# Kernel optimization log

Hardware: AMD Instinct MI355X
Metric: run time of the kernel (lower is better)

Reference implementation:

```python
import jax, jax.numpy as jnp
import numpy as np
import math

B, C_GT, H, W = 32, 1, 256, 1216
SH, SW = 16, 48  # samplesH, samplesW (eval-mode jitter fixed at 0)


def _gauss_kernel():
    # kernel_size = [int(2H/(SH+1)), int(2W/(SW+1))], sigma = size/3 (per original code)
    kh = int(2 * H / (SH + 1))
    kw = int(2 * W / (SW + 1))
    sh = 2 * H / (SH + 1) / 3.0
    sw = 2 * W / (SW + 1) / 3.0
    gh = np.exp(-(((np.arange(kh) - (kh - 1) / 2) / sh) ** 2) / 2) / (sh * math.sqrt(2 * math.pi))
    gw = np.exp(-(((np.arange(kw) - (kw - 1) / 2) / sw) ** 2) / 2) / (sw * math.sqrt(2 * math.pi))
    k = np.outer(gh, gw)
    k = k / k.sum()
    return jnp.asarray(k, jnp.float32)


def _grid_sample_bilinear(img, grid):
    # img [B,C,H,W]; grid [B,Hs,Ws,2] with (x,y) in [-1,1].
    # Matches F.grid_sample(mode='bilinear', padding_mode='zeros', align_corners=False).
    Bb, C, Hh, Ww = img.shape
    x = (grid[..., 0] + 1.0) * Ww / 2.0 - 0.5
    y = (grid[..., 1] + 1.0) * Hh / 2.0 - 0.5
    x0 = jnp.floor(x); y0 = jnp.floor(y)
    x1 = x0 + 1.0;     y1 = y0 + 1.0
    wx1 = x - x0; wx0 = 1.0 - wx1
    wy1 = y - y0; wy0 = 1.0 - wy1
    imt = img.transpose(0, 2, 3, 1)  # [B,H,W,C]
    bidx = jnp.arange(Bb)[:, None, None]

    def gather(yc, xc, wgt):
        m = (yc >= 0) & (yc <= Hh - 1) & (xc >= 0) & (xc <= Ww - 1)
        yi = jnp.clip(yc, 0, Hh - 1).astype(jnp.int32)
        xi = jnp.clip(xc, 0, Ww - 1).astype(jnp.int32)
        v = imt[bidx, yi, xi]  # [B,Hs,Ws,C]
        return v * (wgt * m)[..., None]

    out = (gather(y0, x0, wy0 * wx0) + gather(y0, x1, wy0 * wx1)
           + gather(y1, x0, wy1 * wx0) + gather(y1, x1, wy1 * wx1))
    return out.transpose(0, 3, 1, 2)  # [B,C,Hs,Ws]


def _forward(gt, dense_vector_field):
    # GaussianSmooth: grouped VALID conv with a big separable Gaussian kernel
    k = _gauss_kernel()
    kern = jnp.broadcast_to(k[None, None], (2, 1, k.shape[0], k.shape[1]))
    smoothed = jax.lax.conv_general_dilated(dense_vector_field, kern, (1, 1), 'VALID',
                                            feature_group_count=2)  # [B,2,H',W']
    # F.interpolate(mode='nearest') to (SH, SW): idx = floor(i * in / out)
    hi = np.arange(SH) * smoothed.shape[2] // SH
    wi = np.arange(SW) * smoothed.shape[3] // SW
    svf = smoothed[:, :, hi][:, :, :, wi]  # [B,2,SH,SW]

    # WarpSample base grid (x first, then y — grid_sample convention)
    gw, gh = np.meshgrid(np.linspace(-(SW - 1) / SW, (SW - 1) / SW, SW),
                         np.linspace(-(SH - 1) / SH, (SH - 1) / SH, SH))
    norm_grid = jnp.asarray(np.stack((gw, gh), 2), jnp.float32)  # [SH,SW,2]
    grid_to_sample = svf.transpose(0, 2, 3, 1) + norm_grid  # [B,SH,SW,2]

    gt_sampled = _grid_sample_bilinear(gt, grid_to_sample)  # [B,1,SH,SW]

    # expand(): vectorized scatter replacing the per-pixel Python loop.
    row = jnp.clip(((grid_to_sample[..., 1] + 1.0) / 2.0 * H).astype(jnp.int32), 0, H - 1)
    col = jnp.clip(((grid_to_sample[..., 0] + 1.0) / 2.0 * W).astype(jnp.int32), 0, W - 1)
    bidx = jnp.arange(gt.shape[0])[:, None, None]
    sparse = jnp.zeros((gt.shape[0], H, W, gt.shape[1]), gt.dtype)
    sparse = sparse.at[bidx, row, col].set(gt_sampled.transpose(0, 2, 3, 1))
    sparse = sparse.transpose(0, 3, 1, 2)  # [B,1,H,W]
    # eval-mode KITTI: zero the top 96 rows (no LiDAR returns there)
    sparse = sparse.at[:, :, 0:96, :].set(0.0)
    return sparse, dense_vector_field.transpose(0, 2, 3, 1), grid_to_sample


def setup_inputs():
    key = jax.random.key(0)
    k1, k2 = jax.random.split(key)
    gt = jax.random.uniform(k1, (B, C_GT, H, W), dtype=jnp.float32) * 80.0  # KITTI depth range
    dense_vector_field = jax.random.normal(k2, (B, 2, H, W), dtype=jnp.float32) * 0.1
    return {"gt": gt, "dense_vector_field": dense_vector_field}


def reference(gt, dense_vector_field):
    return _forward(gt, dense_vector_field)
```

## Files before the change

kernel.cpp:

```cpp
#include <hip/hip_runtime.h>
#include <math.h>

#ifndef M_PI
#define M_PI 3.14159265358979323846
#endif

#define Hh   256
#define Ww   1216
#define HWsz (Hh * Ww)
#define Bb   32
#define KH   30
#define KW   49
#define NTAP (KH * KW)
#define SHs  16
#define SWs  48
#define NPB  (SHs * SWs)
#define NPTS (Bb * NPB)
#define OUT0 (Bb * HWsz)
#define OUT1 (Bb * HWsz * 2)

__device__ __forceinline__ float samp4(const float* __restrict__ g, float yc, float xc, float w) {
#pragma clang fp contract(off)
    bool m = (yc >= 0.0f) && (yc <= 255.0f) && (xc >= 0.0f) && (xc <= 1215.0f);
    float ycl = fminf(fmaxf(yc, 0.0f), 255.0f);
    float xcl = fminf(fmaxf(xc, 0.0f), 1215.0f);
    int yi = (int)ycl, xi = (int)xcl;
    float wm = m ? w : 0.0f;
    return g[yi * Ww + xi] * wm;
}

__global__ __launch_bounds__(256) void k_conv_sample(
    const float* __restrict__ gt, const float* __restrict__ dvf,
    float* __restrict__ out2, float* __restrict__ vbuf, int* __restrict__ rcbuf)
{
#pragma clang fp contract(off)
    __shared__ double s_gh[KH];
    __shared__ double s_gw[KW];
    __shared__ double s_S;
    __shared__ float  s_w[NTAP];
    const int tid = threadIdx.x;

    if (tid < KH) {
        const double sh_ = (2.0 * 256.0 / 17.0) / 3.0;
        double u = ((double)tid - 14.5) / sh_;
        s_gh[tid] = exp(-(u * u) / 2.0) / (sh_ * sqrt(2.0 * M_PI));
    } else if (tid >= 64 && tid < 64 + KW) {
        int t = tid - 64;
        const double sw_ = (2.0 * 1216.0 / 49.0) / 3.0;
        double u = ((double)t - 24.0) / sw_;
        s_gw[t] = exp(-(u * u) / 2.0) / (sw_ * sqrt(2.0 * M_PI));
    }
    __syncthreads();
    if (tid == 0) {
        double a = 0.0, c = 0.0;
        for (int t = 0; t < KH; ++t) a += s_gh[t];
        for (int t = 0; t < KW; ++t) c += s_gw[t];
        s_S = a * c;
    }
    __syncthreads();
    for (int t = tid; t < NTAP; t += 256)
        s_w[t] = (float)((s_gh[t / KW] * s_gw[t % KW]) / s_S);
    __syncthreads();

    const int wave = tid >> 6, lane = tid & 63;
    const int pt = blockIdx.x * 4 + wave;
    const int b = pt / NPB, p = pt - b * NPB;
    const int i = p / SWs, j = p - i * SWs;
    const int y0r = (i * 227) >> 4;
    const int x0c = (j * 1168) / 48;
    const float* c0 = dvf + (size_t)b * (2 * HWsz) + y0r * Ww + x0c;
    const float* c1 = c0 + HWsz;

    double a0 = 0.0, a1 = 0.0;
    for (int t = lane; t < NTAP; t += 64) {
        int dy = t / KW, dx = t - dy * KW;
        int off = dy * Ww + dx;
        double w = (double)s_w[t];
        a0 += w * (double)c0[off];
        a1 += w * (double)c1[off];
    }
    for (int o = 32; o > 0; o >>= 1) {
        a0 += __shfl_down(a0, o);
        a1 += __shfl_down(a1, o);
    }

    if (lane == 0) {
        float sx = (float)a0, sy = (float)a1;
        const double startw = -(47.0 / 48.0), stopw = 47.0 / 48.0;
        const double starth = -(15.0 / 16.0), stoph = 15.0 / 16.0;
        const double stepw = (stopw - startw) / 47.0;
        const double steph = (stoph - starth) / 15.0;
        float gwl = (j == SWs - 1) ? (float)stopw : (float)((double)j * stepw + startw);
        float ghl = (i == SHs - 1) ? (float)stoph : (float)((double)i * steph + starth);
        float gx = sx + gwl;
        float gy = sy + ghl;

        float* o2 = out2 + ((size_t)(b * SHs + i) * SWs + j) * 2;
        o2[0] = gx; o2[1] = gy;

        const float* gtb = gt + (size_t)b * HWsz;
        float xw = (gx + 1.0f) * 1216.0f; xw = xw / 2.0f; xw = xw - 0.5f;
        float yw = (gy + 1.0f) * 256.0f;  yw = yw / 2.0f; yw = yw - 0.5f;
        float x0f = floorf(xw), y0f = floorf(yw);
        float x1f = x0f + 1.0f, y1f = y0f + 1.0f;
        float wx1 = xw - x0f, wx0 = 1.0f - wx1;
        float wy1 = yw - y0f, wy0 = 1.0f - wy1;
        float v = samp4(gtb, y0f, x0f, wy0 * wx0) + samp4(gtb, y0f, x1f, wy0 * wx1)
                + samp4(gtb, y1f, x0f, wy1 * wx0) + samp4(gtb, y1f, x1f, wy1 * wx1);

        float rf = (gy + 1.0f) / 2.0f * 256.0f;
        float cf = (gx + 1.0f) / 2.0f * 1216.0f;
        int row = (int)rf; row = row < 0 ? 0 : (row > Hh - 1 ? Hh - 1 : row);
        int col = (int)cf; col = col < 0 ? 0 : (col > Ww - 1 ? Ww - 1 : col);
        vbuf[pt]  = v;
        rcbuf[pt] = (row << 16) | col;
    }
}

__global__ __launch_bounds__(256) void k_scatter(
    const float* __restrict__ vbuf, const int* __restrict__ rcbuf, float* __restrict__ out0)
{
    __shared__ float sv[NPB];
    __shared__ int   sr[NPB];
    const int b = blockIdx.x, tid = threadIdx.x;
    for (int t = tid; t < NPB; t += 256) {
        sv[t] = vbuf[b * NPB + t];
        sr[t] = rcbuf[b * NPB + t];
    }
    __syncthreads();
    if (tid == 0) {
        float* o = out0 + (size_t)b * HWsz;
        for (int p = 0; p < NPB; ++p) {
            int rc = sr[p];
            int r = rc >> 16, c = rc & 0xffff;
            if (r >= 96) o[r * Ww + c] = sv[p];
        }
    }
}

__global__ __launch_bounds__(256) void k_transpose(
    const float* __restrict__ dvf, float* __restrict__ out1)
{
    const size_t idx = (size_t)blockIdx.x * 256 + threadIdx.x;
    const int b = (int)(idx / (HWsz / 4));
    const int r = (int)(idx - (size_t)b * (HWsz / 4));
    const float4* p0 = (const float4*)(dvf + (size_t)b * 2 * HWsz);
    const float4* p1 = (const float4*)(dvf + (size_t)b * 2 * HWsz + HWsz);
    float4 a = p0[r], c = p1[r];
    float4* o = (float4*)(out1 + ((size_t)b * HWsz + (size_t)r * 4) * 2);
    o[0] = make_float4(a.x, c.x, a.y, c.y);
    o[1] = make_float4(a.z, c.z, a.w, c.w);
}

extern "C" void kernel_launch(void* const* d_in, const int* in_sizes, int n_in,
                              void* d_out, int out_size, void* d_ws, size_t ws_size,
                              hipStream_t stream) {
    const float* gt  = (const float*)d_in[0];
    const float* dvf = (const float*)d_in[1];
    float* out0 = (float*)d_out;
    float* out1 = out0 + OUT0;
    float* out2 = out1 + OUT1;
    float* vbuf  = (float*)d_ws;
    int*   rcbuf = (int*)d_ws + NPTS;

    hipMemsetAsync(d_out, 0, (size_t)OUT0 * sizeof(float), stream);
    hipLaunchKernelGGL(k_conv_sample, dim3(NPTS / 4), dim3(256), 0, stream,
                       gt, dvf, out2, vbuf, rcbuf);
    hipLaunchKernelGGL(k_transpose, dim3((Bb * (HWsz / 4)) / 256), dim3(256), 0, stream,
                       dvf, out1);
    hipLaunchKernelGGL(k_scatter, dim3(Bb), dim3(256), 0, stream,
                       vbuf, rcbuf, out0);
}
```

Baseline: 282.9 us.

## Fuse output zeroing into transpose kernel and parallelize scatter with last-writer check

```diff
diff --git a/kernel.cpp b/kernel.cpp
--- a/kernel.cpp
+++ b/kernel.cpp
@@ -36,7 +36,7 @@
 #pragma clang fp contract(off)
     __shared__ double s_gh[KH];
     __shared__ double s_gw[KW];
-    __shared__ double s_S;
+    __shared__ double s_invS;
     __shared__ float  s_w[NTAP];
     const int tid = threadIdx.x;
 
@@ -55,11 +55,14 @@
         double a = 0.0, c = 0.0;
         for (int t = 0; t < KH; ++t) a += s_gh[t];
         for (int t = 0; t < KW; ++t) c += s_gw[t];
-        s_S = a * c;
+        s_invS = 1.0 / (a * c);
     }
     __syncthreads();
-    for (int t = tid; t < NTAP; t += 256)
-        s_w[t] = (float)((s_gh[t / KW] * s_gw[t % KW]) / s_S);
+    {
+        const double invS = s_invS;
+        for (int t = tid; t < NTAP; t += 256)
+            s_w[t] = (float)((s_gh[t / KW] * s_gw[t % KW]) * invS);
+    }
     __syncthreads();
 
     const int wave = tid >> 6, lane = tid & 63;
@@ -128,20 +131,24 @@
         sr[t] = rcbuf[b * NPB + t];
     }
     __syncthreads();
-    if (tid == 0) {
-        float* o = out0 + (size_t)b * HWsz;
-        for (int p = 0; p < NPB; ++p) {
-            int rc = sr[p];
-            int r = rc >> 16, c = rc & 0xffff;
-            if (r >= 96) o[r * Ww + c] = sv[p];
+    float* o = out0 + (size_t)b * HWsz;
+    for (int p = tid; p < NPB; p += 256) {
+        int rc = sr[p];
+        int r = rc >> 16;
+        if (r < 96) continue;
+        bool win = true;
+        for (int q = p + 1; q < NPB; ++q) {
+            if (sr[q] == rc) { win = false; break; }
         }
+        if (win) o[r * Ww + (rc & 0xffff)] = sv[p];
     }
 }
 
-__global__ __launch_bounds__(256) void k_transpose(
-    const float* __restrict__ dvf, float* __restrict__ out1)
+__global__ __launch_bounds__(256) void k_transpose_zero(
+    const float* __restrict__ dvf, float* __restrict__ out1, float* __restrict__ out0)
 {
     const size_t idx = (size_t)blockIdx.x * 256 + threadIdx.x;
+    ((float4*)out0)[idx] = make_float4(0.0f, 0.0f, 0.0f, 0.0f);
     const int b = (int)(idx / (HWsz / 4));
     const int r = (int)(idx - (size_t)b * (HWsz / 4));
     const float4* p0 = (const float4*)(dvf + (size_t)b * 2 * HWsz);
@@ -163,11 +170,10 @@
     float* vbuf  = (float*)d_ws;
     int*   rcbuf = (int*)d_ws + NPTS;
 
-    hipMemsetAsync(d_out, 0, (size_t)OUT0 * sizeof(float), stream);
     hipLaunchKernelGGL(k_conv_sample, dim3(NPTS / 4), dim3(256), 0, stream,
                        gt, dvf, out2, vbuf, rcbuf);
-    hipLaunchKernelGGL(k_transpose, dim3((Bb * (HWsz / 4)) / 256), dim3(256), 0, stream,
-                       dvf, out1);
+    hipLaunchKernelGGL(k_transpose_zero, dim3((Bb * (HWsz / 4)) / 256), dim3(256), 0, stream,
+                       dvf, out1, out0);
     hipLaunchKernelGGL(k_scatter, dim3(Bb), dim3(256), 0, stream,
                        vbuf, rcbuf, out0);
 }
```

After: 298.7 us. 5.6% more time.
